# Kernel tuning notes

Hardware: AMD Instinct MI355X
Metric: run time of the kernel (lower is better)

The kernel has to match this reference:

```python
import jax, jax.numpy as jnp
import numpy as np

N_POINTS = 2_000_000
GRID = 256  # voxel grid resolution (D=H=W), production-scale stand-in for source's 128


def setup_inputs() -> dict:
    key = jax.random.key(0)
    k1, k2, k3 = jax.random.split(key, 3)
    coords = jax.random.uniform(k1, (N_POINTS, 3), dtype=jnp.float32,
                                minval=-0.95, maxval=0.95)
    registration_pred = jax.random.normal(k2, (N_POINTS, 3), dtype=jnp.float32) * 0.02
    registration_gt = jax.random.normal(k3, (N_POINTS, 3), dtype=jnp.float32) * 0.02
    return {"registration_pred": registration_pred,
            "registration_gt": registration_gt,
            "coords": coords}


def _splat(pts, size):
    """Trilinear scatter (adjoint of F.grid_sample, align_corners=False,
    zero padding). pts: [N,3] normalized coords in (x,y,z) order mapping to
    (W,H,D). Splats weight 1 per point. Returns [D,H,W] volume."""
    D = H = W = size
    # grid_sample align_corners=False unnormalization: p = ((g+1)*size - 1)/2
    x = ((pts[:, 0] + 1.0) * W - 1.0) * 0.5
    y = ((pts[:, 1] + 1.0) * H - 1.0) * 0.5
    z = ((pts[:, 2] + 1.0) * D - 1.0) * 0.5
    x0f, y0f, z0f = jnp.floor(x), jnp.floor(y), jnp.floor(z)
    fx, fy, fz = x - x0f, y - y0f, z - z0f  # fractional offsets
    x0, y0, z0 = x0f.astype(jnp.int32), y0f.astype(jnp.int32), z0f.astype(jnp.int32)
    vol = jnp.zeros(D * H * W, dtype=pts.dtype)
    for dz in (0, 1):
        wz = fz if dz else (1.0 - fz)
        for dy in (0, 1):
            wy = fy if dy else (1.0 - fy)
            for dx in (0, 1):
                wx = fx if dx else (1.0 - fx)
                xi, yi, zi = x0 + dx, y0 + dy, z0 + dz
                valid = ((xi >= 0) & (xi < W) & (yi >= 0) & (yi < H)
                         & (zi >= 0) & (zi < D))
                w = jnp.where(valid, wx * wy * wz, 0.0)
                idx = jnp.where(valid, (zi * H + yi) * W + xi, 0)
                vol = vol.at[idx].add(w)
    return vol.reshape(D, H, W)


def reference(registration_pred, registration_gt, coords):
    pred_vol = _splat(coords + registration_pred, GRID)
    gt_vol = _splat(coords + registration_gt, GRID)
    # HuberLoss(reduction='sum', delta=1.0)
    d = pred_vol - gt_vol
    ad = jnp.abs(d)
    return jnp.sum(jnp.where(ad <= 1.0, 0.5 * d * d, ad - 0.5))
```

## Files before the change

### kernel.cpp

```cpp
#include <hip/hip_runtime.h>

#define GRID_RES 256
#define NCELLS 1024
#define CELL_VOX 16384
#define CAP 8192
#define BIN_BLOCKS 256

#define W_SCALE 2097152.0f
#define INV_W (1.0f / 2097152.0f)
#define L_SCALE 512.0f
#define INV_L (1.0f / 512.0f)

template <typename F>
__device__ __forceinline__ void for_each_copy(float px, float py, float pz,
                                              unsigned sign, F&& emit) {
    float x = ((px + 1.0f) * (float)GRID_RES - 1.0f) * 0.5f;
    float y = ((py + 1.0f) * (float)GRID_RES - 1.0f) * 0.5f;
    float z = ((pz + 1.0f) * (float)GRID_RES - 1.0f) * 0.5f;
    float xf = floorf(x), yf = floorf(y), zf = floorf(z);
    int x0 = (int)xf, y0 = (int)yf, z0 = (int)zf;
    unsigned qx = (unsigned)((x - xf) * 65535.0f + 0.5f);
    unsigned qy = (unsigned)((y - yf) * 65535.0f + 0.5f);
    unsigned qz = (unsigned)((z - zf) * 65535.0f + 0.5f);
    unsigned w0 = qx | (qy << 16);

    int cxs[2], cys[2], czs[2];
    int nx = 0, ny = 0, nz = 0;
    {
        bool vA = (x0 >= 0) & (x0 <= 255);
        bool vB = (x0 >= -1) & (x0 <= 254);
        int cA = x0 >> 5, cB = (x0 + 1) >> 5;
        if (vA) cxs[nx++] = cA;
        if (vB && (!vA || cB != cA)) cxs[nx++] = cB;
    }
    {
        bool vA = (y0 >= 0) & (y0 <= 255);
        bool vB = (y0 >= -1) & (y0 <= 254);
        int cA = y0 >> 5, cB = (y0 + 1) >> 5;
        if (vA) cys[ny++] = cA;
        if (vB && (!vA || cB != cA)) cys[ny++] = cB;
    }
    {
        bool vA = (z0 >= 0) & (z0 <= 255);
        bool vB = (z0 >= -1) & (z0 <= 254);
        int cA = z0 >> 4, cB = (z0 + 1) >> 4;
        if (vA) czs[nz++] = cA;
        if (vB && (!vA || cB != cA)) czs[nz++] = cB;
    }
    for (int a = 0; a < nz; ++a) {
        int cz = czs[a];
        unsigned lz = (unsigned)(z0 - (cz << 4) + 1);
        for (int b = 0; b < ny; ++b) {
            int cy = cys[b];
            unsigned ly = (unsigned)(y0 - (cy << 5) + 1);
            for (int c = 0; c < nx; ++c) {
                int cx = cxs[c];
                unsigned lx = (unsigned)(x0 - (cx << 5) + 1);
                int cell = (cz << 6) | (cy << 3) | cx;
                unsigned pack = (lz * 33u + ly) * 33u + lx;
                unsigned w1 = qz | (pack << 16) | (sign << 31);
                emit(cell, w0, w1);
            }
        }
    }
}

__global__ __launch_bounds__(1024) void bin_kernel(
    const float* __restrict__ pred, const float* __restrict__ gt,
    const float* __restrict__ coords, unsigned* __restrict__ gCur,
    uint2* __restrict__ payload, int n) {
    __shared__ unsigned h[NCELLS];
    __shared__ unsigned cur[NCELLS];
    int chunk = (n + gridDim.x - 1) / gridDim.x;
    int start = blockIdx.x * chunk;
    int end = min(start + chunk, n);
    h[threadIdx.x] = 0;
    __syncthreads();

    const float3* c3 = (const float3*)coords;
    const float3* p3 = (const float3*)pred;
    const float3* g3 = (const float3*)gt;

    for (int i = start + (int)threadIdx.x; i < end; i += 1024) {
        float3 c = c3[i];
        float3 p = p3[i];
        float3 g = g3[i];
        for_each_copy(c.x + p.x, c.y + p.y, c.z + p.z, 0u,
                      [&](int cell, unsigned, unsigned) { atomicAdd(&h[cell], 1u); });
        for_each_copy(c.x + g.x, c.y + g.y, c.z + g.z, 1u,
                      [&](int cell, unsigned, unsigned) { atomicAdd(&h[cell], 1u); });
    }
    __syncthreads();

    unsigned cnt = h[threadIdx.x];
    cur[threadIdx.x] = cnt ? atomicAdd(&gCur[threadIdx.x], cnt) : 0u;
    __syncthreads();

    for (int i = start + (int)threadIdx.x; i < end; i += 1024) {
        float3 c = c3[i];
        float3 p = p3[i];
        float3 g = g3[i];
        for_each_copy(c.x + p.x, c.y + p.y, c.z + p.z, 0u,
                      [&](int cell, unsigned w0, unsigned w1) {
                          unsigned slot = atomicAdd(&cur[cell], 1u);
                          if (slot < CAP)
                              payload[((size_t)cell << 13) + slot] = make_uint2(w0, w1);
                      });
        for_each_copy(c.x + g.x, c.y + g.y, c.z + g.z, 1u,
                      [&](int cell, unsigned w0, unsigned w1) {
                          unsigned slot = atomicAdd(&cur[cell], 1u);
                          if (slot < CAP)
                              payload[((size_t)cell << 13) + slot] = make_uint2(w0, w1);
                      });
    }
}

__global__ __launch_bounds__(1024) void accum_kernel(
    const uint2* __restrict__ payload, const unsigned* __restrict__ gCur,
    int* __restrict__ lossAcc) {
    __shared__ int v[CELL_VOX];
    __shared__ float wsum[16];
    int cell = blockIdx.x;
#pragma unroll
    for (int j = 0; j < 16; ++j) v[threadIdx.x + (j << 10)] = 0;
    __syncthreads();

    unsigned cnt = min(gCur[cell], (unsigned)CAP);
    const uint2* pp = payload + ((size_t)cell << 13);
    for (unsigned i = threadIdx.x; i < cnt; i += 1024) {
        uint2 p = pp[i];
        float fx = (float)(p.x & 0xFFFFu) * (1.0f / 65535.0f);
        float fy = (float)(p.x >> 16) * (1.0f / 65535.0f);
        float fz = (float)(p.y & 0xFFFFu) * (1.0f / 65535.0f);
        unsigned pack = (p.y >> 16) & 0x7FFFu;
        unsigned lx = pack % 33u;
        unsigned t = pack / 33u;
        unsigned ly = t % 33u;
        unsigned lz = t / 33u;
        float s = (p.y >> 31) ? -W_SCALE : W_SCALE;
        float wxs[2] = {1.0f - fx, fx};
        float wys[2] = {1.0f - fy, fy};
        float wzs[2] = {1.0f - fz, fz};
        int xb = (int)lx - 1, yb = (int)ly - 1, zb = (int)lz - 1;
#pragma unroll
        for (int dz = 0; dz < 2; ++dz) {
            int rz = zb + dz;
            if ((unsigned)rz > 15u) continue;
            float wz = s * wzs[dz];
#pragma unroll
            for (int dy = 0; dy < 2; ++dy) {
                int ry = yb + dy;
                if ((unsigned)ry > 31u) continue;
                float wyz = wz * wys[dy];
#pragma unroll
                for (int dx = 0; dx < 2; ++dx) {
                    int rx = xb + dx;
                    if ((unsigned)rx > 31u) continue;
                    int iw = __float2int_rn(wyz * wxs[dx]);
                    atomicAdd(&v[(rz << 10) | (ry << 5) | rx], iw);
                }
            }
        }
    }
    __syncthreads();

    float acc = 0.0f;
#pragma unroll
    for (int j = 0; j < 16; ++j) {
        int val = v[threadIdx.x + (j << 10)];
        float d = (float)val * INV_W;
        float ad = fabsf(d);
        acc += (ad <= 1.0f) ? 0.5f * d * d : ad - 0.5f;
    }
#pragma unroll
    for (int off = 32; off > 0; off >>= 1) acc += __shfl_down(acc, off, 64);
    int lane = threadIdx.x & 63;
    int wid = threadIdx.x >> 6;
    if (lane == 0) wsum[wid] = acc;
    __syncthreads();
    if (threadIdx.x == 0) {
        float tsum = 0.0f;
#pragma unroll
        for (int w = 0; w < 16; ++w) tsum += wsum[w];
        atomicAdd(lossAcc, __float2int_rn(tsum * L_SCALE));
    }
}

__global__ void finalize_kernel(const int* __restrict__ lossAcc,
                                float* __restrict__ out) {
    out[0] = (float)lossAcc[0] * INV_L;
}

extern "C" void kernel_launch(void* const* d_in, const int* in_sizes, int n_in,
                              void* d_out, int out_size, void* d_ws, size_t ws_size,
                              hipStream_t stream) {
    const float* reg_pred = (const float*)d_in[0];
    const float* reg_gt   = (const float*)d_in[1];
    const float* coords   = (const float*)d_in[2];
    float* out = (float*)d_out;

    char* ws = (char*)d_ws;
    int* lossAcc = (int*)ws;
    unsigned* gCur = (unsigned*)(ws + 256);
    uint2* payload = (uint2*)(ws + 256 + NCELLS * 4);

    int n = in_sizes[0] / 3;

    hipMemsetAsync(lossAcc, 0, 256 + NCELLS * 4, stream);

    bin_kernel<<<BIN_BLOCKS, 1024, 0, stream>>>(reg_pred, reg_gt, coords,
                                                gCur, payload, n);
    accum_kernel<<<NCELLS, 1024, 0, stream>>>(payload, gCur, lossAcc);
    finalize_kernel<<<1, 1, 0, stream>>>(lossAcc, out);
}
```

Before: 178.5 us.

## Write bin payloads into per-block contiguous segments instead of global per-cell slots

The binning kernel now computes a block-local exclusive scan of per-cell counts and writes each block's records into its own contiguous region, ordered by cell. Per-cell offsets and counts are stored in transposed tables. The accumulate kernel scans the 256 segment counts for its cell and binary-searches to gather records. This removes the global atomic cursor and the scattered writes across 1024 cell buckets, making bin-phase writes more local. In exchange the accumulate reads become gathers from 256 segments, and each thread adds a short binary search.

```diff
diff --git a/kernel.cpp b/kernel.cpp
--- a/kernel.cpp
+++ b/kernel.cpp
@@ -2,9 +2,8 @@
 
 #define GRID_RES 256
 #define NCELLS 1024
-#define CELL_VOX 16384
-#define CAP 8192
-#define BIN_BLOCKS 256
+#define NB 256
+#define BCAP 24576
 
 #define W_SCALE 2097152.0f
 #define INV_W (1.0f / 2097152.0f)
@@ -67,12 +66,14 @@
 
 __global__ __launch_bounds__(1024) void bin_kernel(
     const float* __restrict__ pred, const float* __restrict__ gt,
-    const float* __restrict__ coords, unsigned* __restrict__ gCur,
-    uint2* __restrict__ payload, int n) {
+    const float* __restrict__ coords, unsigned* __restrict__ segOffT,
+    unsigned* __restrict__ segCntT, uint2* __restrict__ payload, int n) {
     __shared__ unsigned h[NCELLS];
     __shared__ unsigned cur[NCELLS];
-    int chunk = (n + gridDim.x - 1) / gridDim.x;
-    int start = blockIdx.x * chunk;
+    __shared__ unsigned wtot[16];
+    int b = blockIdx.x;
+    int chunk = (n + NB - 1) / NB;
+    int start = b * chunk;
     int end = min(start + chunk, n);
     h[threadIdx.x] = 0;
     __syncthreads();
@@ -92,10 +93,29 @@
     }
     __syncthreads();
 
-    unsigned cnt = h[threadIdx.x];
-    cur[threadIdx.x] = cnt ? atomicAdd(&gCur[threadIdx.x], cnt) : 0u;
-    __syncthreads();
-
+    unsigned x = h[threadIdx.x];
+    unsigned incl = x;
+    int lane = threadIdx.x & 63, wid = threadIdx.x >> 6;
+#pragma unroll
+    for (int off = 1; off < 64; off <<= 1) {
+        unsigned y = __shfl_up(incl, off, 64);
+        if (lane >= off) incl += y;
+    }
+    if (lane == 63) wtot[wid] = incl;
+    __syncthreads();
+    if (threadIdx.x == 0) {
+        unsigned r = 0;
+#pragma unroll
+        for (int w = 0; w < 16; ++w) { unsigned v = wtot[w]; wtot[w] = r; r += v; }
+    }
+    __syncthreads();
+    unsigned offE = incl - x + wtot[wid];
+    cur[threadIdx.x] = offE;
+    segOffT[(size_t)threadIdx.x * NB + b] = offE;
+    segCntT[(size_t)threadIdx.x * NB + b] = x;
+    __syncthreads();
+
+    uint2* pb = payload + (size_t)b * BCAP;
     for (int i = start + (int)threadIdx.x; i < end; i += 1024) {
         float3 c = c3[i];
         float3 p = p3[i];
@@ -103,40 +123,73 @@
         for_each_copy(c.x + p.x, c.y + p.y, c.z + p.z, 0u,
                       [&](int cell, unsigned w0, unsigned w1) {
                           unsigned slot = atomicAdd(&cur[cell], 1u);
-                          if (slot < CAP)
-                              payload[((size_t)cell << 13) + slot] = make_uint2(w0, w1);
+                          if (slot < (unsigned)BCAP) pb[slot] = make_uint2(w0, w1);
                       });
         for_each_copy(c.x + g.x, c.y + g.y, c.z + g.z, 1u,
                       [&](int cell, unsigned w0, unsigned w1) {
                           unsigned slot = atomicAdd(&cur[cell], 1u);
-                          if (slot < CAP)
-                              payload[((size_t)cell << 13) + slot] = make_uint2(w0, w1);
+                          if (slot < (unsigned)BCAP) pb[slot] = make_uint2(w0, w1);
                       });
     }
 }
 
 __global__ __launch_bounds__(1024) void accum_kernel(
-    const uint2* __restrict__ payload, const unsigned* __restrict__ gCur,
-    int* __restrict__ lossAcc) {
-    __shared__ int v[CELL_VOX];
+    const uint2* __restrict__ payload, const unsigned* __restrict__ segOffT,
+    const unsigned* __restrict__ segCntT, int* __restrict__ lossAcc) {
+    __shared__ int v[16384];
+    __shared__ unsigned sbase[NB + 1];
+    __shared__ unsigned pbase[NB];
+    __shared__ unsigned w4[4];
     __shared__ float wsum[16];
-    int cell = blockIdx.x;
-#pragma unroll
-    for (int j = 0; j < 16; ++j) v[threadIdx.x + (j << 10)] = 0;
-    __syncthreads();
-
-    unsigned cnt = min(gCur[cell], (unsigned)CAP);
-    const uint2* pp = payload + ((size_t)cell << 13);
-    for (unsigned i = threadIdx.x; i < cnt; i += 1024) {
-        uint2 p = pp[i];
+    int c = blockIdx.x;
+    int t = threadIdx.x;
+#pragma unroll
+    for (int j = 0; j < 16; ++j) v[t + (j << 10)] = 0;
+
+    int lane = t & 63, wid = t >> 6;
+    unsigned cnt = 0, off = 0, incl = 0;
+    if (t < NB) {
+        cnt = segCntT[(size_t)c * NB + t];
+        off = segOffT[(size_t)c * NB + t];
+        incl = cnt;
+#pragma unroll
+        for (int o = 1; o < 64; o <<= 1) {
+            unsigned y = __shfl_up(incl, o, 64);
+            if (lane >= o) incl += y;
+        }
+        if (lane == 63) w4[wid] = incl;
+    }
+    __syncthreads();
+    if (t == 0) {
+        unsigned r = 0;
+#pragma unroll
+        for (int w = 0; w < 4; ++w) { unsigned q = w4[w]; w4[w] = r; r += q; }
+        sbase[NB] = r;
+    }
+    __syncthreads();
+    if (t < NB) {
+        sbase[t] = incl - cnt + w4[wid];
+        pbase[t] = (unsigned)t * (unsigned)BCAP + off;
+    }
+    __syncthreads();
+
+    unsigned total = sbase[NB];
+    for (unsigned i = t; i < total; i += 1024) {
+        int lo = 0, hi = NB - 1;
+#pragma unroll
+        for (int s = 0; s < 8; ++s) {
+            int mid = (lo + hi + 1) >> 1;
+            if (sbase[mid] <= i) lo = mid; else hi = mid - 1;
+        }
+        uint2 p = payload[(size_t)pbase[lo] + (i - sbase[lo])];
         float fx = (float)(p.x & 0xFFFFu) * (1.0f / 65535.0f);
         float fy = (float)(p.x >> 16) * (1.0f / 65535.0f);
         float fz = (float)(p.y & 0xFFFFu) * (1.0f / 65535.0f);
         unsigned pack = (p.y >> 16) & 0x7FFFu;
         unsigned lx = pack % 33u;
-        unsigned t = pack / 33u;
-        unsigned ly = t % 33u;
-        unsigned lz = t / 33u;
+        unsigned tt = pack / 33u;
+        unsigned ly = tt % 33u;
+        unsigned lz = tt / 33u;
         float s = (p.y >> 31) ? -W_SCALE : W_SCALE;
         float wxs[2] = {1.0f - fx, fx};
         float wys[2] = {1.0f - fy, fy};
@@ -167,18 +220,16 @@
     float acc = 0.0f;
 #pragma unroll
     for (int j = 0; j < 16; ++j) {
-        int val = v[threadIdx.x + (j << 10)];
+        int val = v[t + (j << 10)];
         float d = (float)val * INV_W;
         float ad = fabsf(d);
         acc += (ad <= 1.0f) ? 0.5f * d * d : ad - 0.5f;
     }
 #pragma unroll
-    for (int off = 32; off > 0; off >>= 1) acc += __shfl_down(acc, off, 64);
-    int lane = threadIdx.x & 63;
-    int wid = threadIdx.x >> 6;
+    for (int o = 32; o > 0; o >>= 1) acc += __shfl_down(acc, o, 64);
     if (lane == 0) wsum[wid] = acc;
     __syncthreads();
-    if (threadIdx.x == 0) {
+    if (t == 0) {
         float tsum = 0.0f;
 #pragma unroll
         for (int w = 0; w < 16; ++w) tsum += wsum[w];
@@ -201,15 +252,17 @@
 
     char* ws = (char*)d_ws;
     int* lossAcc = (int*)ws;
-    unsigned* gCur = (unsigned*)(ws + 256);
-    uint2* payload = (uint2*)(ws + 256 + NCELLS * 4);
+    unsigned* segOffT = (unsigned*)(ws + 256);
+    unsigned* segCntT = segOffT + (size_t)NCELLS * NB;
+    uint2* payload = (uint2*)((char*)segCntT + (size_t)NCELLS * NB * 4);
 
     int n = in_sizes[0] / 3;
 
-    hipMemsetAsync(lossAcc, 0, 256 + NCELLS * 4, stream);
-
-    bin_kernel<<<BIN_BLOCKS, 1024, 0, stream>>>(reg_pred, reg_gt, coords,
-                                                gCur, payload, n);
-    accum_kernel<<<NCELLS, 1024, 0, stream>>>(payload, gCur, lossAcc);
+    hipMemsetAsync(lossAcc, 0, 256, stream);
+
+    bin_kernel<<<NB, 1024, 0, stream>>>(reg_pred, reg_gt, coords, segOffT,
+                                        segCntT, payload, n);
+    accum_kernel<<<NCELLS, 1024, 0, stream>>>(payload, segOffT, segCntT,
+                                              lossAcc);
     finalize_kernel<<<1, 1, 0, stream>>>(lossAcc, out);
 }
```

New measurement: 183.5 us. +2.8%, slower.
